# Performance work log

Measured on AMD Instinct MI355X. Metric: run time of the kernel, lower is better.

Reference implementation:

```python
import jax, jax.numpy as jnp
import numpy as np
from jax.scipy.special import i0

# NUFFT adjoint (gridding) configuration, matching m_op.plan(uv, (256,256), (512,512), (6,6))
N = 256          # image side
K = 512
J = 6            # kernel support per dim
B = 8            # batch
M = 100000       # n_measurements
ALPHA = K / N    # oversampling = 2
BETA = float(np.pi * np.sqrt((J / ALPHA * (ALPHA - 0.5)) ** 2 - 0.8))  # Fessler KB beta


def setup_inputs() -> dict:
    key = jax.random.key(0)
    k1, k2, k3, k4 = jax.random.split(key, 4)
    y_real = jax.random.normal(k1, (B, M), dtype=jnp.float32)
    y_imag = jax.random.normal(k2, (B, M), dtype=jnp.float32)
    weights = jax.random.uniform(k3, (M,), dtype=jnp.float32, minval=0.1, maxval=1.0)
    uv = jax.random.uniform(k4, (M, 2), dtype=jnp.float32,
                            minval=-np.pi, maxval=np.pi)
    return {"y_real": y_real, "y_imag": y_imag, "weights": weights, "uv": uv}


def _kb(t):
    # Kaiser-Bessel interpolation kernel, support |t| <= J/2
    u = 2.0 * t / J
    return i0(BETA * jnp.sqrt(jnp.clip(1.0 - u * u, 0.0))) / i0(jnp.asarray(BETA, jnp.float32))


def reference(y_real, y_imag, weights, uv):
    # weighted complex measurements: inputs * measurement_weights
    y = (y_real + 1j * y_imag) * weights[None, :]           # (B, M) complex64

    # map uv in [-pi, pi) to oversampled grid coords in [0, K)
    kf = uv * (K / (2.0 * np.pi))                            # (M, 2), DC at index 0 (mod K)
    base = jnp.floor(kf).astype(jnp.int32)                   # (M, 2)
    offs = jnp.arange(-J // 2 + 1, J // 2 + 1)               # [-2..3], 6 taps
    idx = base[:, :, None] + offs[None, None, :]             # (M, 2, J)
    dist = idx.astype(jnp.float32) - kf[:, :, None]
    w = _kb(dist)                                            # (M, 2, J) separable weights
    idxm = jnp.mod(idx, K)                                   # wrap onto torus

    w2 = (w[:, 0, :, None] * w[:, 1, None, :]).reshape(M, J * J)          # (M, 36)
    lin = (idxm[:, 0, :, None] * K + idxm[:, 1, None, :]).reshape(M * J * J)
    vals = (y[:, :, None] * w2[None, :, :].astype(jnp.complex64)).reshape(B, M * J * J)

    # scatter-add onto oversampled Fourier grid
    grid = jnp.zeros((B, K * K), jnp.complex64).at[:, lin].add(vals)
    grid = grid.reshape(B, K, K)

    # inverse FFT, center, crop to N x N
    img = jnp.fft.fftshift(jnp.fft.ifft2(grid), axes=(1, 2))
    c = K // 2
    img = img[:, c - N // 2:c + N // 2, c - N // 2:c + N // 2]

    # deapodization: divide by 1D FT of the KB kernel (always real here since BETA > pi*J/4*... )
    n = jnp.arange(N, dtype=jnp.float32) - N // 2
    xf = np.pi * J * n / K
    arg = BETA * BETA - xf * xf
    d = jnp.sinh(jnp.sqrt(arg)) / jnp.sqrt(arg)              # (N,)
    apod = d[:, None] * d[None, :]

    x = (jnp.real(img) / apod).astype(jnp.float32)           # tf.math.real(adj_op(...))

    # per-image min-max rescale
    tmax = jnp.max(x, axis=(1, 2), keepdims=True)
    tmin = jnp.min(x, axis=(1, 2), keepdims=True)
    return (x - tmin) / (tmax - tmin)
```

## Files before the change

kernel.cpp:

```cpp
#include <hip/hip_runtime.h>
#include <math.h>

#define NN 256
#define KK 512
#define JJ 6
#define BB 8
#define MPTS 100000
#define NBINS (KK * KK)
#define KF_SCALE 81.48733086305615f

typedef _Float16 h8 __attribute__((ext_vector_type(8)));


__device__ __forceinline__ float i0f_dev(float x) {
    float ax = fabsf(x);
    if (ax < 3.75f) {
        float t = x / 3.75f; t *= t;
        return 1.0f + t*(3.5156229f + t*(3.0899424f + t*(1.2067492f +
               t*(0.2659732f + t*(0.0360768f + t*0.0045813f)))));
    } else {
        float t = 3.75f / ax;
        return (expf(ax) * rsqrtf(ax)) *
               (0.39894228f + t*(0.01328592f + t*(0.00225319f + t*(-0.00157565f +
                t*(0.00916281f + t*(-0.02057706f + t*(0.02635537f +
                t*(-0.01647633f + t*0.00392377f))))))));
    }
}

__device__ __forceinline__ float kbf(float t, float beta, float inv_i0b) {
    float u = t * (1.0f / 3.0f);
    float q = fmaxf(1.0f - u * u, 0.0f);
    return i0f_dev(beta * sqrtf(q)) * inv_i0b;
}

__device__ __forceinline__ unsigned fkey(float f) {
    unsigned u = __float_as_uint(f);
    return (u & 0x80000000u) ? ~u : (u | 0x80000000u);
}
__device__ __forceinline__ float funkey(unsigned k) {
    unsigned u = (k & 0x80000000u) ? (k & 0x7FFFFFFFu) : ~k;
    return __uint_as_float(u);
}

__device__ __forceinline__ int wave_scan(int x, int lane) {
#pragma unroll
    for (int off = 1; off < 64; off <<= 1) {
        int y = __shfl_up(x, off, 64);
        if (lane >= off) x += y;
    }
    return x;
}


__global__ __launch_bounds__(256) void count_bins(
    const float2* __restrict__ uv2, int* __restrict__ counts,
    unsigned* __restrict__ mmin, unsigned* __restrict__ mmax)
{
    int m = blockIdx.x * 256 + threadIdx.x;
    if (m < 8) mmin[m] = 0xFFFFFFFFu;
    else if (m < 16) mmax[m - 8] = 0u;
    if (m >= MPTS) return;
    float2 u = uv2[m];
    int b0 = (int)floorf(u.x * KF_SCALE) & (KK - 1);
    int b1 = (int)floorf(u.y * KF_SCALE) & (KK - 1);
    atomicAdd(&counts[(b0 << 9) | b1], 1);
}

__global__ __launch_bounds__(1024) void scan_k(
    const int* __restrict__ counts, int* __restrict__ offsets,
    unsigned long long* __restrict__ desc)
{
    __shared__ int part[16];
    __shared__ int s_prefix;
    int tid = threadIdx.x;
    int lane = tid & 63;
    int w = tid >> 6;
    int g = blockIdx.x * 1024 + tid;

    int v = counts[g];
    int x = wave_scan(v, lane);
    if (lane == 63) part[w] = x;
    __syncthreads();
    if (tid < 16) {
        int p = part[tid];
#pragma unroll
        for (int off = 1; off < 16; off <<= 1) {
            int y = __shfl_up(p, off, 64);
            if (tid >= off) p += y;
        }
        part[tid] = p;
    }
    __syncthreads();
    int incl = x + ((w > 0) ? part[w - 1] : 0);
    int total = part[15];

    if (tid == 0) {
        unsigned long long pack = ((unsigned long long)(unsigned)total << 2) |
                                  ((blockIdx.x == 0) ? 2ULL : 1ULL);
        atomicExch(&desc[blockIdx.x], pack);
        if (blockIdx.x == 0) s_prefix = 0;
    }

    if (blockIdx.x > 0 && w == 0) {
        int prefix = 0;
        int base = blockIdx.x - 1;
        bool done = false;
        while (!done) {
            int idx = base - lane;
            unsigned long long d = 0;
            if (idx >= 0) {
                do { d = atomicAdd(&desc[idx], 0ULL); } while ((d & 3ULL) == 0ULL);
            }
            unsigned long long mask = __ballot(idx >= 0 && (d & 3ULL) == 2ULL);
            int f = (mask != 0ULL) ? (__ffsll((long long)mask) - 1) : 64;
            int contrib = (idx >= 0 && lane <= f) ? (int)(d >> 2) : 0;
#pragma unroll
            for (int off = 1; off < 64; off <<= 1)
                contrib += __shfl_xor(contrib, off, 64);
            prefix += contrib;
            base -= 64;
            done = (mask != 0ULL);
        }
        if (lane == 0) {
            s_prefix = prefix;
            atomicExch(&desc[blockIdx.x],
                       ((unsigned long long)(unsigned)(prefix + total) << 2) | 2ULL);
        }
    }
    __syncthreads();

    offsets[g] = incl - v + s_prefix;
    if (g == 0) offsets[NBINS] = MPTS;
}

__global__ __launch_bounds__(256) void fill_records(
    const float2* __restrict__ uv2,
    const float* __restrict__ y_real, const float* __restrict__ y_imag,
    const float* __restrict__ weights, const int* __restrict__ offsets,
    int* __restrict__ counts, char* __restrict__ rec,
    float beta, float inv_i0b)
{
    int m = blockIdx.x * 256 + threadIdx.x;
    if (m >= MPTS) return;
    float2 u = uv2[m];
    float kf0 = u.x * KF_SCALE;
    float kf1 = u.y * KF_SCALE;
    float f0 = floorf(kf0), f1 = floorf(kf1);
    float fr0 = kf0 - f0, fr1 = kf1 - f1;
    int b1c = (int)f1 & (KK - 1);
    int bin = (((int)f0 & (KK - 1)) << 9) | b1c;
    int old = atomicSub(&counts[bin], 1);
    int slot = offsets[bin] + old - 1;

    _Float16 hw[12];
#pragma unroll
    for (int j = 0; j < JJ; ++j) {
        hw[j]     = (_Float16)kbf((float)(j - 2) - fr0, beta, inv_i0b);
        hw[6 + j] = (_Float16)kbf((float)(j - 2) - fr1, beta, inv_i0b);
    }

    float4 c0v, c1v;
    _Float16* p0 = (_Float16*)&c0v;
    _Float16* p1 = (_Float16*)&c1v;
#pragma unroll
    for (int j = 0; j < 8; ++j) p0[j] = hw[j];
#pragma unroll
    for (int j = 0; j < 4; ++j) p1[j] = hw[8 + j];
    ((int*)&c1v)[2] = b1c;
    ((int*)&c1v)[3] = 0;

    float wm = weights[m];
    h8 ha, hb;
#pragma unroll
    for (int b = 0; b < 4; ++b) {
        ha[2 * b]     = (_Float16)(y_real[b * MPTS + m] * wm);
        ha[2 * b + 1] = (_Float16)(y_imag[b * MPTS + m] * wm);
        hb[2 * b]     = (_Float16)(y_real[(b + 4) * MPTS + m] * wm);
        hb[2 * b + 1] = (_Float16)(y_imag[(b + 4) * MPTS + m] * wm);
    }

    float4* dst = (float4*)(rec + (size_t)slot * 64);
    dst[0] = c0v;
    dst[1] = c1v;
    dst[2] = *(float4*)&ha;
    dst[3] = *(float4*)&hb;
}

__global__ __launch_bounds__(256) void gather_grid(
    const int* __restrict__ offsets, const char* __restrict__ rec,
    float* __restrict__ grid)
{
    __shared__ __align__(16) char lds[4][5120];
    int t = threadIdx.x;
    int lane = t & 63;
    int w = t >> 6;
    int j = blockIdx.x;
    int xcd = j & 7;
    int slot = j >> 3;
    int c0 = (xcd << 6) + (slot >> 1);
    int half = slot & 1;
    int c1base = (half << 8) + (w << 6);
    int c1 = c1base + lane;
    int wa = c1 - 3, wb = c1 + 2;

    char* myl = lds[w];

    float aR[BB], aI[BB];
#pragma unroll
    for (int b = 0; b < BB; ++b) { aR[b] = 0.0f; aI[b] = 0.0f; }

    for (int j0 = 0; j0 < JJ; ++j0) {
        int r0 = (c0 - (j0 - 2)) & (KK - 1);
        int rowbase = r0 << 9;
        int lo = c1base - 3, hi = c1base + 65;
        int nseg, ga0, gb0, ga1, gb1;
        if (lo < 0)        { ga0 = lo; gb0 = -1;  ga1 = 0;   gb1 = hi; nseg = 2; }
        else if (hi > 511) { ga0 = lo; gb0 = 511; ga1 = 512; gb1 = hi; nseg = 2; }
        else               { ga0 = lo; gb0 = hi;  ga1 = 0;   gb1 = 0;  nseg = 1; }

        for (int sgi = 0; sgi < nseg; ++sgi) {
            int ga = sgi ? ga1 : ga0;
            int gb = sgi ? gb1 : gb0;
            int pstart = offsets[rowbase + (ga & 511)];
            int pend   = offsets[rowbase + ((gb & 511) + 1)];
            int ia = max(wa, ga), ib = min(wb, gb);
            bool has = ia <= ib;
            int pA = has ? offsets[rowbase + (ia & 511)] : 0;
            int pB = has ? ((ib == gb) ? pend
                                       : offsets[rowbase + ((ib + 1) & 511)]) : 0;

            for (int pc = pstart; pc < pend; pc += 64) {
                int cnt = min(64, pend - pc);
                int sub = lane & 3;
                int prow = lane >> 2;
#pragma unroll
                for (int q = 0; q < 4; ++q) {
                    if (16 * q < cnt) {
                        int pp = min(pc + prow + 16 * q, MPTS - 1);
                        float4 v = *(const float4*)(rec + (size_t)pp * 64 + sub * 16);
                        *(float4*)(myl + (prow + 16 * q) * 80 + sub * 16) = v;
                    }
                }
                int pLo = max(pA, pc), pHi = min(pB, pc + cnt);
                for (int p = pLo; p < pHi; ++p) {
                    const char* rp = myl + (p - pc) * 80;
                    int bin1 = *(const int*)(rp + 24);
                    int idx = (c1 - bin1 + 2) & 511;
                    bool ok = idx <= 5;
                    idx = ok ? idx : 0;
                    float w0 = (float)*(const _Float16*)(rp + j0 * 2);
                    float w1 = (float)*(const _Float16*)(rp + 12 + idx * 2);
                    float ww = ok ? w0 * w1 : 0.0f;
                    h8 ya = *(const h8*)(rp + 32);
                    h8 yb = *(const h8*)(rp + 48);
#pragma unroll
                    for (int b = 0; b < 4; ++b) {
                        aR[b]     += (float)ya[2 * b]     * ww;
                        aI[b]     += (float)ya[2 * b + 1] * ww;
                        aR[b + 4] += (float)yb[2 * b]     * ww;
                        aI[b + 4] += (float)yb[2 * b + 1] * ww;
                    }
                }
            }
        }
    }

    float2* g2 = (float2*)grid;
    int c = (c0 << 9) + c1;
#pragma unroll
    for (int b = 0; b < BB; ++b)
        g2[((size_t)b << 18) + c] = make_float2(aR[b], aI[b]);
}

__device__ __forceinline__ void wave_fft512(float xr[8], float xi[8], int lane,
                                            const float2* __restrict__ tw)
{
    float a0r = xr[0]+xr[4], a0i = xi[0]+xi[4];
    float a4r = xr[0]-xr[4], a4i = xi[0]-xi[4];
    float a2r = xr[2]+xr[6], a2i = xi[2]+xi[6];
    float a6r = xr[2]-xr[6], a6i = xi[2]-xi[6];
    float a1r = xr[1]+xr[5], a1i = xi[1]+xi[5];
    float a5r = xr[1]-xr[5], a5i = xi[1]-xi[5];
    float a3r = xr[3]+xr[7], a3i = xi[3]+xi[7];
    float a7r = xr[3]-xr[7], a7i = xi[3]-xi[7];
    float b0r = a0r+a2r, b0i = a0i+a2i;
    float b2r = a0r-a2r, b2i = a0i-a2i;
    float b4r = a4r-a6i, b4i = a4i+a6r;
    float b6r = a4r+a6i, b6i = a4i-a6r;
    float b1r = a1r+a3r, b1i = a1i+a3i;
    float b3r = a1r-a3r, b3i = a1i-a3i;
    float b5r = a5r-a7i, b5i = a5i+a7r;
    float b7r = a5r+a7i, b7i = a5i-a7r;
    const float S2 = 0.70710678118654752f;
    float w5r = S2*(b5r-b5i), w5i = S2*(b5r+b5i);
    float w7r = -S2*(b7r+b7i), w7i = S2*(b7r-b7i);
    float y0r = b0r+b1r, y0i = b0i+b1i;
    float y4r = b0r-b1r, y4i = b0i-b1i;
    float y1r = b4r+w5r, y1i = b4i+w5i;
    float y5r = b4r-w5r, y5i = b4i-w5i;
    float y2r = b2r-b3i, y2i = b2i+b3r;
    float y6r = b2r+b3i, y6i = b2i-b3r;
    float y3r = b6r+w7r, y3i = b6i+w7i;
    float y7r = b6r-w7r, y7i = b6i-w7i;

    int p = __brev((unsigned)lane) >> 26;
    float2 w0v = tw[p];
    float c1 = w0v.x, s1 = w0v.y;
    float wr = c1, wi = s1, tr;
    xr[0] = y0r; xi[0] = y0i;
    xr[1] = y1r*wr - y1i*wi; xi[1] = y1i*wr + y1r*wi;
    tr = wr*c1 - wi*s1; wi = wr*s1 + wi*c1; wr = tr;
    xr[2] = y2r*wr - y2i*wi; xi[2] = y2i*wr + y2r*wi;
    tr = wr*c1 - wi*s1; wi = wr*s1 + wi*c1; wr = tr;
    xr[3] = y3r*wr - y3i*wi; xi[3] = y3i*wr + y3r*wi;
    tr = wr*c1 - wi*s1; wi = wr*s1 + wi*c1; wr = tr;
    xr[4] = y4r*wr - y4i*wi; xi[4] = y4i*wr + y4r*wi;
    tr = wr*c1 - wi*s1; wi = wr*s1 + wi*c1; wr = tr;
    xr[5] = y5r*wr - y5i*wi; xi[5] = y5i*wr + y5r*wi;
    tr = wr*c1 - wi*s1; wi = wr*s1 + wi*c1; wr = tr;
    xr[6] = y6r*wr - y6i*wi; xi[6] = y6i*wr + y6r*wi;
    tr = wr*c1 - wi*s1; wi = wr*s1 + wi*c1; wr = tr;
    xr[7] = y7r*wr - y7i*wi; xi[7] = y7i*wr + y7r*wi;

#pragma unroll
    for (int t = 0; t < 6; ++t) {
        int m = 1 << t;
        int j = lane & (m - 1);
        float2 sv = tw[j << (8 - t)];
        float wc = sv.x, wsn = sv.y;
        bool hi = (lane & m) != 0;
#pragma unroll
        for (int d = 0; d < 8; ++d) {
            float pR = __shfl_xor(xr[d], m, 64);
            float pI = __shfl_xor(xi[d], m, 64);
            float bR = hi ? xr[d] : pR;
            float bI = hi ? xi[d] : pI;
            float aR = hi ? pR : xr[d];
            float aI = hi ? pI : xi[d];
            float wbR = wc * bR - wsn * bI;
            float wbI = wc * bI + wsn * bR;
            xr[d] = hi ? aR - wbR : aR + wbR;
            xi[d] = hi ? aI - wbI : aI + wbI;
        }
    }
}

__global__ __launch_bounds__(512) void fftA(
    const float2* __restrict__ grid2, float2* __restrict__ C)
{
    __shared__ float sR[2112], sI[2112];
    __shared__ float2 tw[256];
    int t = threadIdx.x;
    int lane = t & 63;
    int w = t >> 6;
    int b = blockIdx.x & 7;
    int k1base = (blockIdx.x >> 3) << 3;
    int k1 = k1base + w;

    if (t < 256) {
        float ang = (float)(2.0 * M_PI / 512.0) * (float)t;
        float s, c; sincosf(ang, &s, &c);
        tw[t] = make_float2(c, s);
    }

    const float2* row = grid2 + ((size_t)b << 18) + ((size_t)k1 << 9);
    int p = __brev((unsigned)lane) >> 26;
    float xr[8], xi[8];
#pragma unroll
    for (int a = 0; a < 8; ++a) {
        float2 v = row[p + (a << 6)];
        xr[a] = v.x; xi[a] = v.y;
    }
    __syncthreads();

    wave_fft512(xr, xi, lane, tw);

    bool act = (lane < 16) | (lane >= 48);
    int lpp = (lane < 16) ? lane : (lane - 32);
    if (act) {
#pragma unroll
        for (int d = 0; d < 8; ++d) {
            int addr = w * 264 + d * 33 + lpp;
            sR[addr] = xr[d];
            sI[addr] = xi[d];
        }
    }
    __syncthreads();

#pragma unroll
    for (int pp = 0; pp < 4; ++pp) {
        int idx = pp * 512 + t;
        int kk = idx & 7;
        int s2 = idx >> 3;
        int v = (s2 + 128) & 255;
        int d = v & 7;
        int lp = v >> 3;
        int addr = kk * 264 + d * 33 + lp;
        C[(((size_t)(b << 8) + s2) << 9) + k1base + kk] = make_float2(sR[addr], sI[addr]);
    }
}

__global__ __launch_bounds__(256) void fftB(
    const float2* __restrict__ C, float* __restrict__ imgT, float beta2,
    unsigned* __restrict__ mmin, unsigned* __restrict__ mmax)
{
    __shared__ float2 tw[256];
    int t = threadIdx.x;
    int lane = t & 63;
    int w = t >> 6;
    int rowid = blockIdx.x * 4 + w;
    int b = rowid >> 8;
    int s2 = rowid & 255;

    {
        float ang = (float)(2.0 * M_PI / 512.0) * (float)t;
        float s, c; sincosf(ang, &s, &c);
        tw[t] = make_float2(c, s);
    }

    const float2* row = C + ((size_t)rowid << 9);
    int p = __brev((unsigned)lane) >> 26;
    float xr[8], xi[8];
#pragma unroll
    for (int a = 0; a < 8; ++a) {
        float2 v = row[p + (a << 6)];
        xr[a] = v.x; xi[a] = v.y;
    }
    __syncthreads();

    wave_fft512(xr, xi, lane, tw);

    const float XF = (float)(M_PI * (double)JJ / (double)KK);
    const float INVK2 = 1.0f / ((float)KK * (float)KK);
    float ns = (float)(s2 - 128);
    float xfs = XF * ns;
    float asq = beta2 - xfs * xfs;
    float ssq = sqrtf(asq);
    float ds = sinhf(ssq) / ssq;
    float sbase = INVK2 / ds;

    bool act = (lane < 16) | (lane >= 48);
    int lpp = (lane < 16) ? lane : (lane - 32);
    float lmin = 1e30f, lmax = -1e30f;
    if (act) {
        float vals[8];
#pragma unroll
        for (int d = 0; d < 8; ++d) {
            int r = (8 * lpp + d + 128) & 255;
            float nr = (float)(r - 128);
            float xfr = XF * nr;
            float arq = beta2 - xfr * xfr;
            float srq = sqrtf(arq);
            float dr = sinhf(srq) / srq;
            float o = xr[d] * sbase / dr;
            vals[d] = o;
            lmin = fminf(lmin, o);
            lmax = fmaxf(lmax, o);
        }
        int r0run = (8 * lpp + 128) & 255;
        float4* dst = (float4*)(imgT + ((size_t)b << 16) + (s2 << 8) + r0run);
        dst[0] = make_float4(vals[0], vals[1], vals[2], vals[3]);
        dst[1] = make_float4(vals[4], vals[5], vals[6], vals[7]);
    }
#pragma unroll
    for (int off = 32; off >= 1; off >>= 1) {
        lmin = fminf(lmin, __shfl_xor(lmin, off, 64));
        lmax = fmaxf(lmax, __shfl_xor(lmax, off, 64));
    }
    if (lane == 0) {
        atomicMin(&mmin[b], fkey(lmin));
        atomicMax(&mmax[b], fkey(lmax));
    }
}

__global__ __launch_bounds__(256) void norm_t(
    const float* __restrict__ imgT, const unsigned* __restrict__ mmin,
    const unsigned* __restrict__ mmax, float* __restrict__ out)
{
    __shared__ float tile[64][65];
    int b = blockIdx.x >> 4;
    int tl = blockIdx.x & 15;
    int r0 = (tl & 3) << 6;
    int s0 = (tl >> 2) << 6;
    int tr = threadIdx.x & 63;
    int ts = threadIdx.x >> 6;

    const float* src = imgT + ((size_t)b << 16);
#pragma unroll
    for (int q = 0; q < 16; ++q) {
        int s2 = s0 + (q << 2) + ts;
        tile[s2 - s0][tr] = src[(s2 << 8) + r0 + tr];
    }
    __syncthreads();

    float mn = funkey(mmin[b]);
    float inv = 1.0f / (funkey(mmax[b]) - mn);
    float* dst = out + ((size_t)b << 16);
#pragma unroll
    for (int q = 0; q < 16; ++q) {
        int r = r0 + (q << 2) + ts;
        dst[(r << 8) + s0 + tr] = (tile[tr][r - r0] - mn) * inv;
    }
}


static double i0_host(double x) {
    double sum = 1.0, term = 1.0;
    double q = x * x * 0.25;
    for (int k = 1; k < 80; ++k) {
        term *= q / ((double)k * (double)k);
        sum += term;
        if (term < sum * 1e-17) break;
    }
    return sum;
}

extern "C" void kernel_launch(void* const* d_in, const int* in_sizes, int n_in,
                              void* d_out, int out_size, void* d_ws, size_t ws_size,
                              hipStream_t stream)
{
    const float* y_real  = (const float*)d_in[0];
    const float* y_imag  = (const float*)d_in[1];
    const float* weights = (const float*)d_in[2];
    const float2* uv2    = (const float2*)d_in[3];
    float* out = (float*)d_out;

    char* W = (char*)d_ws;
    float*    grid    = (float*)W;
    int*      counts  = (int*)W;
    unsigned long long* desc = (unsigned long long*)(W + 0x100000);
    float*    imgT    = (float*)W;
    char*     A       = W + (size_t)16 * 1024 * 1024;
    char*     rec     = A;
    int*      offsets = (int*)(A + 6400000);
    float2*   C       = (float2*)A;
    unsigned* mmin    = (unsigned*)(A + 8400000);
    unsigned* mmax    = (unsigned*)(A + 8400064);

    double beta_d = M_PI * sqrt(19.45);
    float beta = (float)beta_d;
    float inv_i0b = (float)(1.0 / i0_host(beta_d));
    float beta2 = (float)(beta_d * beta_d);

    hipMemsetAsync(counts, 0, NBINS * sizeof(int) + 256 * sizeof(unsigned long long),
                   stream);

    count_bins<<<(MPTS + 255) / 256, 256, 0, stream>>>(uv2, counts, mmin, mmax);

    scan_k<<<256, 1024, 0, stream>>>(counts, offsets, desc);

    fill_records<<<(MPTS + 255) / 256, 256, 0, stream>>>(
        uv2, y_real, y_imag, weights, offsets, counts, rec, beta, inv_i0b);

    gather_grid<<<1024, 256, 0, stream>>>(offsets, rec, grid);

    fftA<<<512, 512, 0, stream>>>((const float2*)grid, C);

    fftB<<<512, 256, 0, stream>>>(C, imgT, beta2, mmin, mmax);

    norm_t<<<128, 256, 0, stream>>>(imgT, mmin, mmax, out);
}
```

Before: 159.9 us.

## Split gather batch across half-waves and use KB lookup table in fill

The gather kernel now assigns each 64-lane wave 32 grid columns, with the two half-waves each accumulating four of the eight batch images. This halves per-thread accumulators and the per-wave LDS staging window, and doubles the grid to 2048 blocks. Separately, the Kaiser-Bessel weights in fill_records are now read from a 1024-entry table, built in count_bins and linearly interpolated, instead of evaluating the Bessel function per tap. The table trades a small loss of accuracy for fewer transcendental evaluations. The gather change repeats the same point scans for more columns, which adds redundant loads and offset lookups.

New measurement: 169.5 us. +6.0%, slower.

```diff
diff --git a/kernel.cpp b/kernel.cpp
--- a/kernel.cpp
+++ b/kernel.cpp
@@ -51,14 +51,28 @@
     return x;
 }
 
+__device__ __forceinline__ float kb_lut(const float* __restrict__ sT, float t) {
+    float u = (t + 3.0f) * (1023.0f / 6.0f);
+    int i = (int)u;
+    i = min(i, 1022);
+    float f = u - (float)i;
+    float a = sT[i];
+    return a + f * (sT[i + 1] - sT[i]);
+}
+
 
 __global__ __launch_bounds__(256) void count_bins(
     const float2* __restrict__ uv2, int* __restrict__ counts,
-    unsigned* __restrict__ mmin, unsigned* __restrict__ mmax)
+    unsigned* __restrict__ mmin, unsigned* __restrict__ mmax,
+    float* __restrict__ lut, float beta, float inv_i0b)
 {
     int m = blockIdx.x * 256 + threadIdx.x;
     if (m < 8) mmin[m] = 0xFFFFFFFFu;
     else if (m < 16) mmax[m - 8] = 0u;
+    if (m < 1024) {
+        float t = -3.0f + (6.0f / 1023.0f) * (float)m;
+        lut[m] = kbf(t, beta, inv_i0b);
+    }
     if (m >= MPTS) return;
     float2 u = uv2[m];
     int b0 = (int)floorf(u.x * KF_SCALE) & (KK - 1);
@@ -138,9 +152,15 @@
     const float* __restrict__ y_real, const float* __restrict__ y_imag,
     const float* __restrict__ weights, const int* __restrict__ offsets,
     int* __restrict__ counts, char* __restrict__ rec,
-    float beta, float inv_i0b)
-{
-    int m = blockIdx.x * 256 + threadIdx.x;
+    const float* __restrict__ lut)
+{
+    __shared__ float sT[1024];
+    int tid = threadIdx.x;
+#pragma unroll
+    for (int q = 0; q < 4; ++q) sT[q * 256 + tid] = lut[q * 256 + tid];
+    __syncthreads();
+
+    int m = blockIdx.x * 256 + tid;
     if (m >= MPTS) return;
     float2 u = uv2[m];
     float kf0 = u.x * KF_SCALE;
@@ -155,8 +175,8 @@
     _Float16 hw[12];
 #pragma unroll
     for (int j = 0; j < JJ; ++j) {
-        hw[j]     = (_Float16)kbf((float)(j - 2) - fr0, beta, inv_i0b);
-        hw[6 + j] = (_Float16)kbf((float)(j - 2) - fr1, beta, inv_i0b);
+        hw[j]     = (_Float16)kb_lut(sT, (float)(j - 2) - fr0);
+        hw[6 + j] = (_Float16)kb_lut(sT, (float)(j - 2) - fr1);
     }
 
     float4 c0v, c1v;
@@ -190,29 +210,30 @@
     const int* __restrict__ offsets, const char* __restrict__ rec,
     float* __restrict__ grid)
 {
-    __shared__ __align__(16) char lds[4][5120];
+    __shared__ __align__(16) char lds[4][2816];
     int t = threadIdx.x;
     int lane = t & 63;
     int w = t >> 6;
+    int half = lane >> 5;
+    int l32 = lane & 31;
     int j = blockIdx.x;
     int xcd = j & 7;
-    int slot = j >> 3;
-    int c0 = (xcd << 6) + (slot >> 1);
-    int half = slot & 1;
-    int c1base = (half << 8) + (w << 6);
-    int c1 = c1base + lane;
+    int c0 = (xcd << 6) + ((j >> 3) & 63);
+    int q4 = j >> 9;
+    int c1base = (q4 << 7) + (w << 5);
+    int c1 = c1base + l32;
     int wa = c1 - 3, wb = c1 + 2;
 
     char* myl = lds[w];
 
-    float aR[BB], aI[BB];
-#pragma unroll
-    for (int b = 0; b < BB; ++b) { aR[b] = 0.0f; aI[b] = 0.0f; }
+    float aR[4], aI[4];
+#pragma unroll
+    for (int b = 0; b < 4; ++b) { aR[b] = 0.0f; aI[b] = 0.0f; }
 
     for (int j0 = 0; j0 < JJ; ++j0) {
         int r0 = (c0 - (j0 - 2)) & (KK - 1);
         int rowbase = r0 << 9;
-        int lo = c1base - 3, hi = c1base + 65;
+        int lo = c1base - 3, hi = c1base + 33;
         int nseg, ga0, gb0, ga1, gb1;
         if (lo < 0)        { ga0 = lo; gb0 = -1;  ga1 = 0;   gb1 = hi; nseg = 2; }
         else if (hi > 511) { ga0 = lo; gb0 = 511; ga1 = 512; gb1 = hi; nseg = 2; }
@@ -229,21 +250,21 @@
             int pB = has ? ((ib == gb) ? pend
                                        : offsets[rowbase + ((ib + 1) & 511)]) : 0;
 
-            for (int pc = pstart; pc < pend; pc += 64) {
-                int cnt = min(64, pend - pc);
+            for (int pc = pstart; pc < pend; pc += 32) {
+                int cnt = min(32, pend - pc);
                 int sub = lane & 3;
                 int prow = lane >> 2;
 #pragma unroll
-                for (int q = 0; q < 4; ++q) {
-                    if (16 * q < cnt) {
-                        int pp = min(pc + prow + 16 * q, MPTS - 1);
+                for (int qq = 0; qq < 2; ++qq) {
+                    if (16 * qq < cnt) {
+                        int pp = min(pc + prow + 16 * qq, MPTS - 1);
                         float4 v = *(const float4*)(rec + (size_t)pp * 64 + sub * 16);
-                        *(float4*)(myl + (prow + 16 * q) * 80 + sub * 16) = v;
+                        *(float4*)(myl + (prow + 16 * qq) * 88 + sub * 16) = v;
                     }
                 }
                 int pLo = max(pA, pc), pHi = min(pB, pc + cnt);
                 for (int p = pLo; p < pHi; ++p) {
-                    const char* rp = myl + (p - pc) * 80;
+                    const char* rp = myl + (p - pc) * 88;
                     int bin1 = *(const int*)(rp + 24);
                     int idx = (c1 - bin1 + 2) & 511;
                     bool ok = idx <= 5;
@@ -251,14 +272,11 @@
                     float w0 = (float)*(const _Float16*)(rp + j0 * 2);
                     float w1 = (float)*(const _Float16*)(rp + 12 + idx * 2);
                     float ww = ok ? w0 * w1 : 0.0f;
-                    h8 ya = *(const h8*)(rp + 32);
-                    h8 yb = *(const h8*)(rp + 48);
+                    h8 yv = *(const h8*)(rp + 32 + (half << 4));
 #pragma unroll
                     for (int b = 0; b < 4; ++b) {
-                        aR[b]     += (float)ya[2 * b]     * ww;
-                        aI[b]     += (float)ya[2 * b + 1] * ww;
-                        aR[b + 4] += (float)yb[2 * b]     * ww;
-                        aI[b + 4] += (float)yb[2 * b + 1] * ww;
+                        aR[b] += (float)yv[2 * b]     * ww;
+                        aI[b] += (float)yv[2 * b + 1] * ww;
                     }
                 }
             }
@@ -268,8 +286,8 @@
     float2* g2 = (float2*)grid;
     int c = (c0 << 9) + c1;
 #pragma unroll
-    for (int b = 0; b < BB; ++b)
-        g2[((size_t)b << 18) + c] = make_float2(aR[b], aI[b]);
+    for (int b = 0; b < 4; ++b)
+        g2[((size_t)((half << 2) + b) << 18) + c] = make_float2(aR[b], aI[b]);
 }
 
 __device__ __forceinline__ void wave_fft512(float xr[8], float xi[8], int lane,
@@ -536,6 +554,7 @@
     float2*   C       = (float2*)A;
     unsigned* mmin    = (unsigned*)(A + 8400000);
     unsigned* mmax    = (unsigned*)(A + 8400064);
+    float*    lut     = (float*)(A + 8400128);
 
     double beta_d = M_PI * sqrt(19.45);
     float beta = (float)beta_d;
@@ -545,14 +564,15 @@
     hipMemsetAsync(counts, 0, NBINS * sizeof(int) + 256 * sizeof(unsigned long long),
                    stream);
 
-    count_bins<<<(MPTS + 255) / 256, 256, 0, stream>>>(uv2, counts, mmin, mmax);
+    count_bins<<<(MPTS + 255) / 256, 256, 0, stream>>>(
+        uv2, counts, mmin, mmax, lut, beta, inv_i0b);
 
     scan_k<<<256, 1024, 0, stream>>>(counts, offsets, desc);
 
     fill_records<<<(MPTS + 255) / 256, 256, 0, stream>>>(
-        uv2, y_real, y_imag, weights, offsets, counts, rec, beta, inv_i0b);
-
-    gather_grid<<<1024, 256, 0, stream>>>(offsets, rec, grid);
+        uv2, y_real, y_imag, weights, offsets, counts, rec, lut);
+
+    gather_grid<<<2048, 256, 0, stream>>>(offsets, rec, grid);
 
     fftA<<<512, 512, 0, stream>>>((const float2*)grid, C);
 
```
